# Performance work log

Measured on AMD Instinct MI355X. Metric: run time of the kernel, lower is better.

The kernel has to match this reference:

```python
import jax, jax.numpy as jnp
import numpy as np

E = 512
H = 8
D = E // H  # head_dim = 64
SCALE = D ** -0.5
NEG_INF = float('-inf')


def layer_norm(x, g, b, eps=1e-5):
    mu = jnp.mean(x, axis=-1, keepdims=True)
    var = jnp.var(x, axis=-1, keepdims=True)
    return (x - mu) * jax.lax.rsqrt(var + eps) * g + b


def setup_inputs() -> dict:
    key = jax.random.key(0)
    ks = jax.random.split(key, 16)
    B, Q, K = 4, 2048, 2048
    inp = {
        'query': jax.random.normal(ks[0], (B, Q, E), jnp.float32),
        'key_value': jax.random.normal(ks[1], (B, K, E), jnp.float32),
        'kv_mask': jax.random.randint(ks[2], (B, K), 0, 2) > 0,
        'sparse_mask': jax.random.randint(ks[3], (B, Q, K), 0, 2) > 0,
        'ln_q_g': jnp.ones((E,), jnp.float32),
        'ln_q_b': jnp.zeros((E,), jnp.float32),
        'ln_kv_g': jnp.ones((E,), jnp.float32),
        'ln_kv_b': jnp.zeros((E,), jnp.float32),
        # Linear weights stored as (in, out): y = x @ W + b
        'Wq': jax.random.normal(ks[4], (E, E), jnp.float32) * (E ** -0.5),
        'bq': jnp.zeros((E,), jnp.float32),
        'Wk': jax.random.normal(ks[5], (E, E), jnp.float32) * (E ** -0.5),
        'bk': jnp.zeros((E,), jnp.float32),
        'Wv': jax.random.normal(ks[6], (E, E), jnp.float32) * (E ** -0.5),
        'bv': jnp.zeros((E,), jnp.float32),
        'Wo': jax.random.normal(ks[7], (E, E), jnp.float32) * (E ** -0.5),
        'bo': jnp.zeros((E,), jnp.float32),
    }
    return inp


def reference(query, key_value, kv_mask, sparse_mask,
              ln_q_g, ln_q_b, ln_kv_g, ln_kv_b,
              Wq, bq, Wk, bk, Wv, bv, Wo, bo):
    B, Qn, _ = query.shape
    Kn = key_value.shape[1]
    qn = layer_norm(query, ln_q_g, ln_q_b)
    kvn = layer_norm(key_value, ln_kv_g, ln_kv_b)
    q = (qn @ Wq + bq).reshape(B, Qn, H, D)
    k = (kvn @ Wk + bk).reshape(B, Kn, H, D)
    v = (kvn @ Wv + bv).reshape(B, Kn, H, D)
    # scores: [B, H, Q, K]
    scores = jnp.einsum('bqhd,bkhd->bhqk', q, k) * SCALE
    mask = kv_mask[:, None, None, :] & sparse_mask[:, None, :, :]
    scores = jnp.where(mask, scores, NEG_INF)
    attn = jax.nn.softmax(scores, axis=-1)
    # nan_to_num(0): rows with no valid key -> all-zero weights
    valid_row = jnp.any(mask, axis=-1, keepdims=True)
    attn = jnp.where(valid_row, attn, 0.0)
    out = jnp.einsum('bhqk,bkhd->bqhd', attn, v).reshape(B, Qn, E)
    return out @ Wo + bo
```

## Files before the change

### kernel.cpp

```cpp
#include <hip/hip_runtime.h>
#include <hip/hip_bf16.h>
#include <math.h>

typedef unsigned short ushort_t;
typedef __attribute__((ext_vector_type(8))) __bf16 bf16x8;
typedef __attribute__((ext_vector_type(4))) float f32x4;
typedef __attribute__((ext_vector_type(16))) float f32x16;
typedef __attribute__((ext_vector_type(4))) unsigned int u32x4;

#define E_DIM 512
#define HEADS 8
#define HD 64
#define SEQ 2048
#define NROWS 8192
#define QSCALE 0.18033688011112042f

static __device__ __forceinline__ unsigned short f2b(float f) {
  unsigned int x;
  __builtin_memcpy(&x, &f, 4);
  x += 0x7fffu + ((x >> 16) & 1u);
  return (unsigned short)(x >> 16);
}

static __device__ __forceinline__ unsigned cvt_pk_bf16(float lo, float hi) {
  unsigned r;
  asm("v_cvt_pk_bf16_f32 %0, %1, %2" : "=v"(r) : "v"(lo), "v"(hi));
  return r;
}

static __device__ __forceinline__ float fexp2(float x) {
  float r;
  asm("v_exp_f32 %0, %1" : "=v"(r) : "v"(x));
  return r;
}

static __device__ __forceinline__ unsigned bitmask1(unsigned v, int off) {
#if __has_builtin(__builtin_amdgcn_sbfe)
  return (unsigned)__builtin_amdgcn_sbfe((int)v, off, 1);
#else
  return (unsigned)((int)(v << (31 - off)) >> 31);
#endif
}

static __device__ __forceinline__ int swz(int row, int col) {
  return row * 64 + ((((col >> 3) ^ (row & 7)) & 7) << 3) + (col & 7);
}

static __device__ __forceinline__ void gl2lds16(const ushort_t* g, ushort_t* s) {
#if __has_builtin(__builtin_amdgcn_global_load_lds)
  __builtin_amdgcn_global_load_lds(
      (const __attribute__((address_space(1))) unsigned int*)(uintptr_t)g,
      (__attribute__((address_space(3))) unsigned int*)(uintptr_t)s,
      16, 0, 0);
#else
  int l = threadIdx.x & 63;
  *(u32x4*)(s + l * 8) = *(const u32x4*)g;
#endif
}

__launch_bounds__(256)
__global__ void prep_kernel(const float* __restrict__ Wq, const float* __restrict__ Wk,
                            const float* __restrict__ Wv, const float* __restrict__ Wo,
                            ushort_t* __restrict__ WT,
                            const int* __restrict__ kvm, const int* __restrict__ sp,
                            unsigned long long* __restrict__ bits,
                            const float* __restrict__ xq, const float* __restrict__ xkv,
                            const float* __restrict__ gq, const float* __restrict__ bq,
                            const float* __restrict__ gkv, const float* __restrict__ bkv,
                            ushort_t* __restrict__ yq, ushort_t* __restrict__ ykv) {
  int blk = blockIdx.x;
  int t = threadIdx.x;
  if (blk < 1024) {
    int z = blk >> 8, rem = blk & 255;
    const float* in = (z == 0) ? Wq : (z == 1) ? Wk : (z == 2) ? Wv : Wo;
    ushort_t* o = WT + (size_t)z * E_DIM * E_DIM;
    __shared__ float tile[32 * 33];
    int tx = t & 31, ty = t >> 5;
    int n0 = (rem & 15) * 32, k0 = (rem >> 4) * 32;
#pragma unroll
    for (int i = 0; i < 4; ++i) {
      int k = ty + i * 8;
      tile[k * 33 + tx] = in[(k0 + k) * E_DIM + n0 + tx];
    }
    __syncthreads();
#pragma unroll
    for (int i = 0; i < 4; ++i) {
      int n = ty + i * 8;
      o[(n0 + n) * E_DIM + k0 + tx] = f2b(tile[tx * 33 + n]);
    }
  } else if (blk < 3072) {
    int w = t >> 6, l = t & 63;
    int row = (blk - 1024) * 4 + w;
    int b = row >> 11;
    const int4* sprow = (const int4*)(sp + ((size_t)row << 11));
    const int4* kvrow = (const int4*)(kvm + ((size_t)b << 11));
    unsigned long long* out = bits + ((size_t)row << 5);
#pragma unroll
    for (int it = 0; it < 8; ++it) {
      int4 s4 = sprow[it * 64 + l];
      int4 k4 = kvrow[it * 64 + l];
      unsigned nib = (unsigned)((s4.x && k4.x) ? 1 : 0) | ((s4.y && k4.y) ? 2u : 0)
                   | ((s4.z && k4.z) ? 4u : 0) | ((s4.w && k4.w) ? 8u : 0);
      unsigned long long b0 = __ballot((nib & 1u) != 0);
      unsigned long long b1 = __ballot((nib & 2u) != 0);
      unsigned long long b2 = __ballot((nib & 4u) != 0);
      unsigned long long b3 = __ballot((nib & 8u) != 0);
      if (l < 4) {
        int m16 = l * 16;
        unsigned long long wv = ((b0 >> m16) & 0xFFFFull)
                              | (((b1 >> m16) & 0xFFFFull) << 16)
                              | (((b2 >> m16) & 0xFFFFull) << 32)
                              | (((b3 >> m16) & 0xFFFFull) << 48);
        out[it * 4 + l] = wv;
      }
    }
  } else {
    int idx = blk - 3072;
    int which = idx >> 11;
    const float* x = which ? xkv : xq;
    const float* g = which ? gkv : gq;
    const float* bb = which ? bkv : bq;
    ushort_t* y = which ? ykv : yq;
    int w = t >> 6, l = t & 63;
    int row = (idx & 2047) * 4 + w;
    f32x4 x0 = *(const f32x4*)&x[row * E_DIM + l * 8];
    f32x4 x1 = *(const f32x4*)&x[row * E_DIM + l * 8 + 4];
    float xf[8], s = 0.f, ss = 0.f;
#pragma unroll
    for (int j = 0; j < 8; ++j) {
      xf[j] = (j < 4) ? x0[j] : x1[j - 4];
      s += xf[j];
      ss += xf[j] * xf[j];
    }
#pragma unroll
    for (int off = 32; off > 0; off >>= 1) {
      s += __shfl_xor(s, off);
      ss += __shfl_xor(ss, off);
    }
    float mu = s * (1.f / 512.f);
    float var = fmaxf(ss * (1.f / 512.f) - mu * mu, 0.f);
    float rs = rsqrtf(var + 1e-5f);
    f32x4 g0 = *(const f32x4*)&g[l * 8];
    f32x4 g1 = *(const f32x4*)&g[l * 8 + 4];
    f32x4 b0 = *(const f32x4*)&bb[l * 8];
    f32x4 b1 = *(const f32x4*)&bb[l * 8 + 4];
#pragma unroll
    for (int j = 0; j < 8; ++j) {
      float gv = (j < 4) ? g0[j] : g1[j - 4];
      float bv = (j < 4) ? b0[j] : b1[j - 4];
      y[row * E_DIM + l * 8 + j] = f2b((xf[j] - mu) * rs * gv + bv);
    }
  }
}

template <int MODE>
static __device__ __forceinline__ void gemm_core64(ushort_t* lA, ushort_t* lB,
                                                   const ushort_t* __restrict__ A,
                                                   const ushort_t* __restrict__ WT,
                                                   const float* __restrict__ bias,
                                                   void* Cv, float scale, int m0, int n0) {
  int t = threadIdx.x, w = t >> 6, l = t & 63;
  int quad = l >> 4, l15 = l & 15;
  int wm_ = w >> 1, wn_ = w & 1;
  int csrc = ((l & 7) ^ (l >> 3)) * 8;
  int rln = l >> 3;

  f32x4 acc[4][2] = {};
  for (int kk = 0; kk < E_DIM; kk += 64) {
    __syncthreads();
#pragma unroll
    for (int i = 0; i < 4; ++i) {
      int r0 = i * 32 + w * 8;
      gl2lds16(&A[(size_t)(m0 + r0 + rln) * E_DIM + kk + csrc], &lA[r0 * 64]);
    }
#pragma unroll
    for (int i = 0; i < 2; ++i) {
      int r0 = i * 32 + w * 8;
      gl2lds16(&WT[(size_t)(n0 + r0 + rln) * E_DIM + kk + csrc], &lB[r0 * 64]);
    }
    __syncthreads();
#pragma unroll
    for (int ks = 0; ks < 2; ++ks) {
      bf16x8 af[4], bf[2];
#pragma unroll
      for (int mt = 0; mt < 4; ++mt)
        af[mt] = *(const bf16x8*)&lA[swz(wm_ * 64 + mt * 16 + l15, ks * 32 + quad * 8)];
#pragma unroll
      for (int nt = 0; nt < 2; ++nt)
        bf[nt] = *(const bf16x8*)&lB[swz(wn_ * 32 + nt * 16 + l15, ks * 32 + quad * 8)];
#pragma unroll
      for (int mt = 0; mt < 4; ++mt)
#pragma unroll
        for (int nt = 0; nt < 2; ++nt)
          acc[mt][nt] = __builtin_amdgcn_mfma_f32_16x16x32_bf16(af[mt], bf[nt], acc[mt][nt], 0, 0, 0);
    }
  }

#pragma unroll
  for (int nt = 0; nt < 2; ++nt) {
    int col = n0 + wn_ * 32 + nt * 16 + l15;
    float bv = bias[col];
    if constexpr (MODE == 2) {
      int h = col >> 6, d = col & 63;
#pragma unroll
      for (int mt = 0; mt < 4; ++mt) {
        int row = m0 + wm_ * 64 + mt * 16 + quad * 4;
        int b = row >> 11, k = row & 2047;
        union { ushort_t u[4]; uint2 v; } pk;
#pragma unroll
        for (int r = 0; r < 4; ++r) pk.u[r] = f2b(acc[mt][nt][r] + bv);
        *(uint2*)&((ushort_t*)Cv)[((((size_t)(b * HEADS + h)) * HD + d) << 11) + k] = pk.v;
      }
    } else {
#pragma unroll
      for (int mt = 0; mt < 4; ++mt) {
#pragma unroll
        for (int r = 0; r < 4; ++r) {
          int rowm = m0 + wm_ * 64 + mt * 16 + quad * 4 + r;
          float val = (acc[mt][nt][r] + bv) * scale;
          if constexpr (MODE == 0)
            ((ushort_t*)Cv)[rowm * E_DIM + col] = f2b(val);
          else
            ((float*)Cv)[rowm * E_DIM + col] = val;
        }
      }
    }
  }
}

__launch_bounds__(256)
__global__ void proj3_kernel(const ushort_t* __restrict__ qn, const ushort_t* __restrict__ WTq,
                             const float* __restrict__ bq, ushort_t* __restrict__ qp,
                             const ushort_t* __restrict__ kvn, const ushort_t* __restrict__ WTv,
                             const float* __restrict__ bv, ushort_t* __restrict__ Vt,
                             const ushort_t* __restrict__ WTk, const float* __restrict__ bk,
                             ushort_t* __restrict__ kp, int zbase) {
  __shared__ ushort_t lA[128 * 64];
  __shared__ ushort_t lB[64 * 64];
  int flat = blockIdx.x;
  int chunk = gridDim.x >> 3;
  int work = (flat & 7) * chunk + (flat >> 3);
  int z = zbase + (work >> 9);
  int r = work & 511;
  int m0 = (r >> 3) * 128, n0 = (r & 7) * 64;
  if (z == 0)      gemm_core64<0>(lA, lB, qn,  WTq, bq, qp, QSCALE, m0, n0);
  else if (z == 1) gemm_core64<2>(lA, lB, kvn, WTv, bv, Vt, 1.f,    m0, n0);
  else             gemm_core64<0>(lA, lB, kvn, WTk, bk, kp, 1.f,    m0, n0);
}

__launch_bounds__(256)
__global__ void out_kernel(const ushort_t* __restrict__ A, const ushort_t* __restrict__ WT,
                           const float* __restrict__ bias, float* __restrict__ C) {
  __shared__ ushort_t lA[128 * 64];
  __shared__ ushort_t lB[64 * 64];
  int flat = blockIdx.x;
  int work = (flat & 7) * 64 + (flat >> 3);
  int m0 = (work >> 3) * 128, n0 = (work & 7) * 64;
  gemm_core64<1>(lA, lB, A, WT, bias, C, 1.f, m0, n0);
}

static __device__ __forceinline__ void softmax_frag(const f32x16& s0, const f32x16& s1,
                                                    unsigned mlo, unsigned mhi, int half,
                                                    bf16x8* pf, f32x16* dummy_unused) {
#pragma unroll
  for (int kt2 = 0; kt2 < 2; ++kt2) {
    const f32x16& sv = kt2 ? s1 : s0;
    unsigned wa[4], wb[4];
#pragma unroll
    for (int g = 0; g < 4; ++g) {
      int bb = 8 * kt2 + 2 * g + half;
      unsigned q0u = __float_as_uint(fexp2(sv[g * 4 + 0])) & bitmask1(mlo, bb);
      unsigned q1u = __float_as_uint(fexp2(sv[g * 4 + 1])) & bitmask1(mlo, bb + 16);
      unsigned q2u = __float_as_uint(fexp2(sv[g * 4 + 2])) & bitmask1(mhi, bb);
      unsigned q3u = __float_as_uint(fexp2(sv[g * 4 + 3])) & bitmask1(mhi, bb + 16);
      wa[g] = cvt_pk_bf16(__uint_as_float(q0u), __uint_as_float(q1u));
      wb[g] = cvt_pk_bf16(__uint_as_float(q2u), __uint_as_float(q3u));
    }
    asm("v_permlane32_swap_b32 %0, %1" : "+v"(wa[0]), "+v"(wa[1]));
    asm("v_permlane32_swap_b32 %0, %1" : "+v"(wb[0]), "+v"(wb[1]));
    asm("v_permlane32_swap_b32 %0, %1" : "+v"(wa[2]), "+v"(wa[3]));
    asm("v_permlane32_swap_b32 %0, %1" : "+v"(wb[2]), "+v"(wb[3]));
    union { unsigned u[4]; bf16x8 v; } f0, f1;
    f0.u[0] = wa[0]; f0.u[1] = wb[0]; f0.u[2] = wa[1]; f0.u[3] = wb[1];
    f1.u[0] = wa[2]; f1.u[1] = wb[2]; f1.u[2] = wa[3]; f1.u[3] = wb[3];
    pf[kt2 * 2 + 0] = f0.v;
    pf[kt2 * 2 + 1] = f1.v;
  }
}

__launch_bounds__(256)
__global__ void attn_kernel(const ushort_t* __restrict__ Qp, const ushort_t* __restrict__ Kp,
                            const ushort_t* __restrict__ Vt,
                            const unsigned long long* __restrict__ bits,
                            ushort_t* __restrict__ ctx) {
  __shared__ __align__(16) char smemb[73728];
  ushort_t* sQ = (ushort_t*)smemb;
  int t = threadIdx.x, w = t >> 6, l = t & 63;
  int qw = w & 1, ks = w >> 1;
  ushort_t* sKA = (ushort_t*)(smemb + 8192 + ks * 16384);
  ushort_t* sKB = sKA + 4096;
  ushort_t* sVA = (ushort_t*)(smemb + 40960 + ks * 16384);
  ushort_t* sVB = sVA + 4096;
  int l31 = l & 31, half = l >> 5;

  int flat = blockIdx.x;
  int work = (flat & 7) * 128 + (flat >> 3);
  int qblk = work & 31;
  int h = (work >> 5) & 7;
  int b = work >> 8;
  int q0 = qblk * 64;
  int bh = b * HEADS + h;
  int myq = qw * 32 + l31;
  int csrc = ((l & 7) ^ (l >> 3)) * 8;
  int rln = l >> 3;

#pragma unroll
  for (int it = 0; it < 2; ++it) {
    int r0 = w * 16 + it * 8;
    gl2lds16(&Qp[(size_t)(b * SEQ + q0 + r0 + rln) * E_DIM + h * HD + csrc], &sQ[r0 * 64]);
  }
  __syncthreads();
  bf16x8 qf[4];
#pragma unroll
  for (int ds = 0; ds < 4; ++ds)
    qf[ds] = *(const bf16x8*)&sQ[swz(myq, ds * 16 + 8 * half)];

  const unsigned long long* mrow = bits + ((size_t)(b * SEQ + q0 + myq) << 5);
  f32x16 o0 = {}, o1 = {}, lacc = {};
  union { unsigned u[4]; bf16x8 v; } onec;
#pragma unroll
  for (int i = 0; i < 4; ++i) onec.u[i] = 0x3f803f80u;

  for (int t8 = 0; t8 < 8; ++t8) {
    int ktA = t8 * 4 + ks * 2;
    int kA0 = ktA * 64, kB0 = kA0 + 64;
    unsigned long long mA = mrow[ktA], mB = mrow[ktA + 1];
    __syncthreads();
#pragma unroll
    for (int it = 0; it < 4; ++it) {
      int r0 = (it * 2 + qw) * 8;
      gl2lds16(&Kp[(size_t)(b * SEQ + kA0 + r0 + rln) * E_DIM + h * HD + csrc], &sKA[r0 * 64]);
      gl2lds16(&Kp[(size_t)(b * SEQ + kB0 + r0 + rln) * E_DIM + h * HD + csrc], &sKB[r0 * 64]);
      gl2lds16(&Vt[((size_t)bh * HD + r0 + rln) * SEQ + kA0 + csrc], &sVA[r0 * 64]);
      gl2lds16(&Vt[((size_t)bh * HD + r0 + rln) * SEQ + kB0 + csrc], &sVB[r0 * 64]);
    }
    __syncthreads();

    f32x16 sA0 = {}, sA1 = {}, sB0 = {}, sB1 = {};
    __builtin_amdgcn_s_setprio(1);
#pragma unroll
    for (int ds = 0; ds < 4; ++ds) {
      bf16x8 kfA0 = *(const bf16x8*)&sKA[swz(l31, ds * 16 + 8 * half)];
      bf16x8 kfA1 = *(const bf16x8*)&sKA[swz(32 + l31, ds * 16 + 8 * half)];
      bf16x8 kfB0 = *(const bf16x8*)&sKB[swz(l31, ds * 16 + 8 * half)];
      bf16x8 kfB1 = *(const bf16x8*)&sKB[swz(32 + l31, ds * 16 + 8 * half)];
      sA0 = __builtin_amdgcn_mfma_f32_32x32x16_bf16(kfA0, qf[ds], sA0, 0, 0, 0);
      sA1 = __builtin_amdgcn_mfma_f32_32x32x16_bf16(kfA1, qf[ds], sA1, 0, 0, 0);
      sB0 = __builtin_amdgcn_mfma_f32_32x32x16_bf16(kfB0, qf[ds], sB0, 0, 0, 0);
      sB1 = __builtin_amdgcn_mfma_f32_32x32x16_bf16(kfB1, qf[ds], sB1, 0, 0, 0);
    }
    __builtin_amdgcn_s_setprio(0);

    bf16x8 pfA[4], pfB[4];
    softmax_frag(sA0, sA1, (unsigned)mA, (unsigned)(mA >> 32), half, pfA, nullptr);
    softmax_frag(sB0, sB1, (unsigned)mB, (unsigned)(mB >> 32), half, pfB, nullptr);

    __builtin_amdgcn_s_setprio(1);
#pragma unroll
    for (int ksp = 0; ksp < 4; ++ksp) {
      bf16x8 vfA0 = *(const bf16x8*)&sVA[swz(l31, ksp * 16 + 8 * half)];
      bf16x8 vfA1 = *(const bf16x8*)&sVA[swz(32 + l31, ksp * 16 + 8 * half)];
      o0 = __builtin_amdgcn_mfma_f32_32x32x16_bf16(vfA0, pfA[ksp], o0, 0, 0, 0);
      o1 = __builtin_amdgcn_mfma_f32_32x32x16_bf16(vfA1, pfA[ksp], o1, 0, 0, 0);
      lacc = __builtin_amdgcn_mfma_f32_32x32x16_bf16(onec.v, pfA[ksp], lacc, 0, 0, 0);
      bf16x8 vfB0 = *(const bf16x8*)&sVB[swz(l31, ksp * 16 + 8 * half)];
      bf16x8 vfB1 = *(const bf16x8*)&sVB[swz(32 + l31, ksp * 16 + 8 * half)];
      o0 = __builtin_amdgcn_mfma_f32_32x32x16_bf16(vfB0, pfB[ksp], o0, 0, 0, 0);
      o1 = __builtin_amdgcn_mfma_f32_32x32x16_bf16(vfB1, pfB[ksp], o1, 0, 0, 0);
      lacc = __builtin_amdgcn_mfma_f32_32x32x16_bf16(onec.v, pfB[ksp], lacc, 0, 0, 0);
    }
    __builtin_amdgcn_s_setprio(0);
  }

  float lsum = lacc[0];

  __syncthreads();
  float* mrg = (float*)(smemb + 8192);
  if (ks == 1) {
    float* e = mrg + (qw * 64 + l) * 33;
#pragma unroll
    for (int r = 0; r < 16; ++r) e[r] = o0[r];
#pragma unroll
    for (int r = 0; r < 16; ++r) e[16 + r] = o1[r];
    e[32] = lsum;
  }
  __syncthreads();
  if (ks == 0) {
    const float* e = mrg + (qw * 64 + l) * 33;
#pragma unroll
    for (int r = 0; r < 16; ++r) o0[r] += e[r];
#pragma unroll
    for (int r = 0; r < 16; ++r) o1[r] += e[16 + r];
    lsum += e[32];
    float inv = (lsum > 0.f) ? 1.f / lsum : 0.f;
    size_t base = (size_t)(b * SEQ + q0 + myq) * E_DIM + h * HD;
#pragma unroll
    for (int dt = 0; dt < 2; ++dt) {
      const f32x16& oo = dt ? o1 : o0;
#pragma unroll
      for (int g = 0; g < 4; ++g) {
        union { ushort_t u[4]; uint2 v; } ov;
#pragma unroll
        for (int r = 0; r < 4; ++r) ov.u[r] = f2b(oo[g * 4 + r] * inv);
        *(uint2*)&ctx[base + dt * 32 + g * 8 + 4 * half] = ov.v;
      }
    }
  }
}

extern "C" void kernel_launch(void* const* d_in, const int* in_sizes, int n_in,
                              void* d_out, int out_size, void* d_ws, size_t ws_size,
                              hipStream_t stream) {
  const float* query     = (const float*)d_in[0];
  const float* key_value = (const float*)d_in[1];
  const int*   kv_mask   = (const int*)d_in[2];
  const int*   sp_mask   = (const int*)d_in[3];
  const float* ln_q_g  = (const float*)d_in[4];
  const float* ln_q_b  = (const float*)d_in[5];
  const float* ln_kv_g = (const float*)d_in[6];
  const float* ln_kv_b = (const float*)d_in[7];
  const float* Wq = (const float*)d_in[8];
  const float* bq = (const float*)d_in[9];
  const float* Wk = (const float*)d_in[10];
  const float* bk = (const float*)d_in[11];
  const float* Wv = (const float*)d_in[12];
  const float* bv = (const float*)d_in[13];
  const float* Wo = (const float*)d_in[14];
  const float* bo = (const float*)d_in[15];

  const size_t NB = (size_t)NROWS * E_DIM;
  char* ws = (char*)d_ws;
  ushort_t* bufA = (ushort_t*)ws;
  ushort_t* bufB = bufA + NB;
  ushort_t* WT   = bufB + NB;
  ushort_t* WTq = WT;
  ushort_t* WTk = WTq + E_DIM * E_DIM;
  ushort_t* WTv = WTk + E_DIM * E_DIM;
  ushort_t* WTo = WTv + E_DIM * E_DIM;
  unsigned long long* bits = (unsigned long long*)(WTo + E_DIM * E_DIM);
  ushort_t* bufC = (ushort_t*)(ws + (20u << 20));

  ushort_t* dlo = (ushort_t*)d_out;
  ushort_t* dhi = dlo + NB;

  bool fused = ws_size >= (28u << 20);
  ushort_t* kp = fused ? bufC : dlo;

  prep_kernel<<<7168, 256, 0, stream>>>(Wq, Wk, Wv, Wo, WT, kv_mask, sp_mask, bits,
                                        query, key_value, ln_q_g, ln_q_b, ln_kv_g, ln_kv_b,
                                        dlo, bufA);

  if (fused) {
    proj3_kernel<<<1536, 256, 0, stream>>>(dlo, WTq, bq, dhi,
                                           bufA, WTv, bv, bufB,
                                           WTk, bk, bufC, 0);
  } else {
    proj3_kernel<<<1024, 256, 0, stream>>>(dlo, WTq, bq, dhi,
                                           bufA, WTv, bv, bufB,
                                           WTk, bk, dlo, 0);
    proj3_kernel<<<512, 256, 0, stream>>>(dlo, WTq, bq, dhi,
                                          bufA, WTv, bv, bufB,
                                          WTk, bk, dlo, 2);
  }

  attn_kernel<<<1024, 256, 0, stream>>>(dhi, kp, bufB, bits, bufA);

  out_kernel<<<512, 256, 0, stream>>>(bufA, WTo, bo, (float*)d_out);
}
```

Baseline: 244.5 us.

## Move mask bit-packing into projection GEMM launch to overlap with compute

Mask packing (the sparse and kv masks turned into per-row bitmasks) moves out of the prep kernel and into the projection GEMM kernel. Its blocks are interleaved with GEMM blocks in groups (4 mask blocks per 3 GEMM blocks in the fused path), so the memory-bound mask reads can overlap with MFMA-bound GEMM work. The prep kernel shrinks to weight transpose and layernorm. The cost is a more complex block-index mapping in the projection kernel and possible tile-scheduling and L2-locality effects from mixing the two kinds of work.

```diff
diff --git a/kernel.cpp b/kernel.cpp
--- a/kernel.cpp
+++ b/kernel.cpp
@@ -62,8 +62,6 @@
 __global__ void prep_kernel(const float* __restrict__ Wq, const float* __restrict__ Wk,
                             const float* __restrict__ Wv, const float* __restrict__ Wo,
                             ushort_t* __restrict__ WT,
-                            const int* __restrict__ kvm, const int* __restrict__ sp,
-                            unsigned long long* __restrict__ bits,
                             const float* __restrict__ xq, const float* __restrict__ xkv,
                             const float* __restrict__ gq, const float* __restrict__ bq,
                             const float* __restrict__ gkv, const float* __restrict__ bkv,
@@ -88,9 +86,139 @@
       int n = ty + i * 8;
       o[(n0 + n) * E_DIM + k0 + tx] = f2b(tile[tx * 33 + n]);
     }
-  } else if (blk < 3072) {
+  } else {
+    int idx = blk - 1024;
+    int which = idx >> 11;
+    const float* x = which ? xkv : xq;
+    const float* g = which ? gkv : gq;
+    const float* bb = which ? bkv : bq;
+    ushort_t* y = which ? ykv : yq;
     int w = t >> 6, l = t & 63;
-    int row = (blk - 1024) * 4 + w;
+    int row = (idx & 2047) * 4 + w;
+    f32x4 x0 = *(const f32x4*)&x[row * E_DIM + l * 8];
+    f32x4 x1 = *(const f32x4*)&x[row * E_DIM + l * 8 + 4];
+    float xf[8], s = 0.f, ss = 0.f;
+#pragma unroll
+    for (int j = 0; j < 8; ++j) {
+      xf[j] = (j < 4) ? x0[j] : x1[j - 4];
+      s += xf[j];
+      ss += xf[j] * xf[j];
+    }
+#pragma unroll
+    for (int off = 32; off > 0; off >>= 1) {
+      s += __shfl_xor(s, off);
+      ss += __shfl_xor(ss, off);
+    }
+    float mu = s * (1.f / 512.f);
+    float var = fmaxf(ss * (1.f / 512.f) - mu * mu, 0.f);
+    float rs = rsqrtf(var + 1e-5f);
+    f32x4 g0 = *(const f32x4*)&g[l * 8];
+    f32x4 g1 = *(const f32x4*)&g[l * 8 + 4];
+    f32x4 b0 = *(const f32x4*)&bb[l * 8];
+    f32x4 b1 = *(const f32x4*)&bb[l * 8 + 4];
+#pragma unroll
+    for (int j = 0; j < 8; ++j) {
+      float gv = (j < 4) ? g0[j] : g1[j - 4];
+      float bv = (j < 4) ? b0[j] : b1[j - 4];
+      y[row * E_DIM + l * 8 + j] = f2b((xf[j] - mu) * rs * gv + bv);
+    }
+  }
+}
+
+template <int MODE>
+static __device__ __forceinline__ void gemm_core64(ushort_t* lA, ushort_t* lB,
+                                                   const ushort_t* __restrict__ A,
+                                                   const ushort_t* __restrict__ WT,
+                                                   const float* __restrict__ bias,
+                                                   void* Cv, float scale, int m0, int n0) {
+  int t = threadIdx.x, w = t >> 6, l = t & 63;
+  int quad = l >> 4, l15 = l & 15;
+  int wm_ = w >> 1, wn_ = w & 1;
+  int csrc = ((l & 7) ^ (l >> 3)) * 8;
+  int rln = l >> 3;
+
+  f32x4 acc[4][2] = {};
+  for (int kk = 0; kk < E_DIM; kk += 64) {
+    __syncthreads();
+#pragma unroll
+    for (int i = 0; i < 4; ++i) {
+      int r0 = i * 32 + w * 8;
+      gl2lds16(&A[(size_t)(m0 + r0 + rln) * E_DIM + kk + csrc], &lA[r0 * 64]);
+    }
+#pragma unroll
+    for (int i = 0; i < 2; ++i) {
+      int r0 = i * 32 + w * 8;
+      gl2lds16(&WT[(size_t)(n0 + r0 + rln) * E_DIM + kk + csrc], &lB[r0 * 64]);
+    }
+    __syncthreads();
+#pragma unroll
+    for (int ks = 0; ks < 2; ++ks) {
+      bf16x8 af[4], bf[2];
+#pragma unroll
+      for (int mt = 0; mt < 4; ++mt)
+        af[mt] = *(const bf16x8*)&lA[swz(wm_ * 64 + mt * 16 + l15, ks * 32 + quad * 8)];
+#pragma unroll
+      for (int nt = 0; nt < 2; ++nt)
+        bf[nt] = *(const bf16x8*)&lB[swz(wn_ * 32 + nt * 16 + l15, ks * 32 + quad * 8)];
+#pragma unroll
+      for (int mt = 0; mt < 4; ++mt)
+#pragma unroll
+        for (int nt = 0; nt < 2; ++nt)
+          acc[mt][nt] = __builtin_amdgcn_mfma_f32_16x16x32_bf16(af[mt], bf[nt], acc[mt][nt], 0, 0, 0);
+    }
+  }
+
+#pragma unroll
+  for (int nt = 0; nt < 2; ++nt) {
+    int col = n0 + wn_ * 32 + nt * 16 + l15;
+    float bv = bias[col];
+    if constexpr (MODE == 2) {
+      int h = col >> 6, d = col & 63;
+#pragma unroll
+      for (int mt = 0; mt < 4; ++mt) {
+        int row = m0 + wm_ * 64 + mt * 16 + quad * 4;
+        int b = row >> 11, k = row & 2047;
+        union { ushort_t u[4]; uint2 v; } pk;
+#pragma unroll
+        for (int r = 0; r < 4; ++r) pk.u[r] = f2b(acc[mt][nt][r] + bv);
+        *(uint2*)&((ushort_t*)Cv)[((((size_t)(b * HEADS + h)) * HD + d) << 11) + k] = pk.v;
+      }
+    } else {
+#pragma unroll
+      for (int mt = 0; mt < 4; ++mt) {
+#pragma unroll
+        for (int r = 0; r < 4; ++r) {
+          int rowm = m0 + wm_ * 64 + mt * 16 + quad * 4 + r;
+          float val = (acc[mt][nt][r] + bv) * scale;
+          if constexpr (MODE == 0)
+            ((ushort_t*)Cv)[rowm * E_DIM + col] = f2b(val);
+          else
+            ((float*)Cv)[rowm * E_DIM + col] = val;
+        }
+      }
+    }
+  }
+}
+
+__launch_bounds__(256)
+__global__ void proj3_kernel(const ushort_t* __restrict__ qn, const ushort_t* __restrict__ WTq,
+                             const float* __restrict__ bq, ushort_t* __restrict__ qp,
+                             const ushort_t* __restrict__ kvn, const ushort_t* __restrict__ WTv,
+                             const float* __restrict__ bv, ushort_t* __restrict__ Vt,
+                             const ushort_t* __restrict__ WTk, const float* __restrict__ bk,
+                             ushort_t* __restrict__ kp,
+                             const int* __restrict__ kvm, const int* __restrict__ sp,
+                             unsigned long long* __restrict__ bits,
+                             int nm, int ng, int ngemm, int zbase) {
+  __shared__ ushort_t lA[128 * 64];
+  __shared__ ushort_t lB[64 * 64];
+  int flat = blockIdx.x;
+  int gsz = nm + ng;
+  int grp = flat / gsz, r = flat % gsz;
+  if (r < nm) {
+    int mb = grp * nm + r;
+    int w = threadIdx.x >> 6, l = threadIdx.x & 63;
+    int row = mb * 4 + w;
     int b = row >> 11;
     const int4* sprow = (const int4*)(sp + ((size_t)row << 11));
     const int4* kvrow = (const int4*)(kvm + ((size_t)b << 11));
@@ -114,135 +242,14 @@
         out[it * 4 + l] = wv;
       }
     }
-  } else {
-    int idx = blk - 3072;
-    int which = idx >> 11;
-    const float* x = which ? xkv : xq;
-    const float* g = which ? gkv : gq;
-    const float* bb = which ? bkv : bq;
-    ushort_t* y = which ? ykv : yq;
-    int w = t >> 6, l = t & 63;
-    int row = (idx & 2047) * 4 + w;
-    f32x4 x0 = *(const f32x4*)&x[row * E_DIM + l * 8];
-    f32x4 x1 = *(const f32x4*)&x[row * E_DIM + l * 8 + 4];
-    float xf[8], s = 0.f, ss = 0.f;
-#pragma unroll
-    for (int j = 0; j < 8; ++j) {
-      xf[j] = (j < 4) ? x0[j] : x1[j - 4];
-      s += xf[j];
-      ss += xf[j] * xf[j];
-    }
-#pragma unroll
-    for (int off = 32; off > 0; off >>= 1) {
-      s += __shfl_xor(s, off);
-      ss += __shfl_xor(ss, off);
-    }
-    float mu = s * (1.f / 512.f);
-    float var = fmaxf(ss * (1.f / 512.f) - mu * mu, 0.f);
-    float rs = rsqrtf(var + 1e-5f);
-    f32x4 g0 = *(const f32x4*)&g[l * 8];
-    f32x4 g1 = *(const f32x4*)&g[l * 8 + 4];
-    f32x4 b0 = *(const f32x4*)&bb[l * 8];
-    f32x4 b1 = *(const f32x4*)&bb[l * 8 + 4];
-#pragma unroll
-    for (int j = 0; j < 8; ++j) {
-      float gv = (j < 4) ? g0[j] : g1[j - 4];
-      float bv = (j < 4) ? b0[j] : b1[j - 4];
-      y[row * E_DIM + l * 8 + j] = f2b((xf[j] - mu) * rs * gv + bv);
-    }
-  }
-}
-
-template <int MODE>
-static __device__ __forceinline__ void gemm_core64(ushort_t* lA, ushort_t* lB,
-                                                   const ushort_t* __restrict__ A,
-                                                   const ushort_t* __restrict__ WT,
-                                                   const float* __restrict__ bias,
-                                                   void* Cv, float scale, int m0, int n0) {
-  int t = threadIdx.x, w = t >> 6, l = t & 63;
-  int quad = l >> 4, l15 = l & 15;
-  int wm_ = w >> 1, wn_ = w & 1;
-  int csrc = ((l & 7) ^ (l >> 3)) * 8;
-  int rln = l >> 3;
-
-  f32x4 acc[4][2] = {};
-  for (int kk = 0; kk < E_DIM; kk += 64) {
-    __syncthreads();
-#pragma unroll
-    for (int i = 0; i < 4; ++i) {
-      int r0 = i * 32 + w * 8;
-      gl2lds16(&A[(size_t)(m0 + r0 + rln) * E_DIM + kk + csrc], &lA[r0 * 64]);
-    }
-#pragma unroll
-    for (int i = 0; i < 2; ++i) {
-      int r0 = i * 32 + w * 8;
-      gl2lds16(&WT[(size_t)(n0 + r0 + rln) * E_DIM + kk + csrc], &lB[r0 * 64]);
-    }
-    __syncthreads();
-#pragma unroll
-    for (int ks = 0; ks < 2; ++ks) {
-      bf16x8 af[4], bf[2];
-#pragma unroll
-      for (int mt = 0; mt < 4; ++mt)
-        af[mt] = *(const bf16x8*)&lA[swz(wm_ * 64 + mt * 16 + l15, ks * 32 + quad * 8)];
-#pragma unroll
-      for (int nt = 0; nt < 2; ++nt)
-        bf[nt] = *(const bf16x8*)&lB[swz(wn_ * 32 + nt * 16 + l15, ks * 32 + quad * 8)];
-#pragma unroll
-      for (int mt = 0; mt < 4; ++mt)
-#pragma unroll
-        for (int nt = 0; nt < 2; ++nt)
-          acc[mt][nt] = __builtin_amdgcn_mfma_f32_16x16x32_bf16(af[mt], bf[nt], acc[mt][nt], 0, 0, 0);
-    }
-  }
-
-#pragma unroll
-  for (int nt = 0; nt < 2; ++nt) {
-    int col = n0 + wn_ * 32 + nt * 16 + l15;
-    float bv = bias[col];
-    if constexpr (MODE == 2) {
-      int h = col >> 6, d = col & 63;
-#pragma unroll
-      for (int mt = 0; mt < 4; ++mt) {
-        int row = m0 + wm_ * 64 + mt * 16 + quad * 4;
-        int b = row >> 11, k = row & 2047;
-        union { ushort_t u[4]; uint2 v; } pk;
-#pragma unroll
-        for (int r = 0; r < 4; ++r) pk.u[r] = f2b(acc[mt][nt][r] + bv);
-        *(uint2*)&((ushort_t*)Cv)[((((size_t)(b * HEADS + h)) * HD + d) << 11) + k] = pk.v;
-      }
-    } else {
-#pragma unroll
-      for (int mt = 0; mt < 4; ++mt) {
-#pragma unroll
-        for (int r = 0; r < 4; ++r) {
-          int rowm = m0 + wm_ * 64 + mt * 16 + quad * 4 + r;
-          float val = (acc[mt][nt][r] + bv) * scale;
-          if constexpr (MODE == 0)
-            ((ushort_t*)Cv)[rowm * E_DIM + col] = f2b(val);
-          else
-            ((float*)Cv)[rowm * E_DIM + col] = val;
-        }
-      }
-    }
-  }
-}
-
-__launch_bounds__(256)
-__global__ void proj3_kernel(const ushort_t* __restrict__ qn, const ushort_t* __restrict__ WTq,
-                             const float* __restrict__ bq, ushort_t* __restrict__ qp,
-                             const ushort_t* __restrict__ kvn, const ushort_t* __restrict__ WTv,
-                             const float* __restrict__ bv, ushort_t* __restrict__ Vt,
-                             const ushort_t* __restrict__ WTk, const float* __restrict__ bk,
-                             ushort_t* __restrict__ kp, int zbase) {
-  __shared__ ushort_t lA[128 * 64];
-  __shared__ ushort_t lB[64 * 64];
-  int flat = blockIdx.x;
-  int chunk = gridDim.x >> 3;
-  int work = (flat & 7) * chunk + (flat >> 3);
+    return;
+  }
+  int gid = grp * ng + (r - nm);
+  int chunk = ngemm >> 3;
+  int work = (gid & 7) * chunk + (gid >> 3);
   int z = zbase + (work >> 9);
-  int r = work & 511;
-  int m0 = (r >> 3) * 128, n0 = (r & 7) * 64;
+  int rr = work & 511;
+  int m0 = (rr >> 3) * 128, n0 = (rr & 7) * 64;
   if (z == 0)      gemm_core64<0>(lA, lB, qn,  WTq, bq, qp, QSCALE, m0, n0);
   else if (z == 1) gemm_core64<2>(lA, lB, kvn, WTv, bv, Vt, 1.f,    m0, n0);
   else             gemm_core64<0>(lA, lB, kvn, WTk, bk, kp, 1.f,    m0, n0);
@@ -456,21 +463,27 @@
   bool fused = ws_size >= (28u << 20);
   ushort_t* kp = fused ? bufC : dlo;
 
-  prep_kernel<<<7168, 256, 0, stream>>>(Wq, Wk, Wv, Wo, WT, kv_mask, sp_mask, bits,
+  prep_kernel<<<5120, 256, 0, stream>>>(Wq, Wk, Wv, Wo, WT,
                                         query, key_value, ln_q_g, ln_q_b, ln_kv_g, ln_kv_b,
                                         dlo, bufA);
 
   if (fused) {
-    proj3_kernel<<<1536, 256, 0, stream>>>(dlo, WTq, bq, dhi,
+    proj3_kernel<<<3584, 256, 0, stream>>>(dlo, WTq, bq, dhi,
                                            bufA, WTv, bv, bufB,
-                                           WTk, bk, bufC, 0);
+                                           WTk, bk, bufC,
+                                           kv_mask, sp_mask, bits,
+                                           4, 3, 1536, 0);
   } else {
-    proj3_kernel<<<1024, 256, 0, stream>>>(dlo, WTq, bq, dhi,
+    proj3_kernel<<<3072, 256, 0, stream>>>(dlo, WTq, bq, dhi,
                                            bufA, WTv, bv, bufB,
-                                           WTk, bk, dlo, 0);
+                                           WTk, bk, dlo,
+                                           kv_mask, sp_mask, bits,
+                                           2, 1, 1024, 0);
     proj3_kernel<<<512, 256, 0, stream>>>(dlo, WTq, bq, dhi,
                                           bufA, WTv, bv, bufB,
-                                          WTk, bk, dlo, 2);
+                                          WTk, bk, dlo,
+                                          kv_mask, sp_mask, bits,
+                                          0, 1, 512, 2);
   }
 
   attn_kernel<<<1024, 256, 0, stream>>>(dhi, kp, bufB, bits, bufA);
```

Measured after the change: 259.4 us. 1.06x slower.
